# Performance work log

Hardware: AMD Instinct MI355X
Metric: run time of the kernel (lower is better)

Reference implementation:

```python
import jax, jax.numpy as jnp
import numpy as np

HIDDEN = 64
NHEADS = 8
HEAD_DIM = HIDDEN // NHEADS
N_EDGES = 800000
N_NODES = 50000


def setup_inputs() -> dict:
    key = jax.random.key(0)
    k1, k2, k3, k4 = jax.random.split(key, 4)
    keys = jax.random.normal(k1, (N_EDGES, HIDDEN), dtype=jnp.float32)
    queries = jax.random.normal(k2, (N_EDGES, HIDDEN), dtype=jnp.float32)
    values = jax.random.normal(k3, (N_EDGES, HIDDEN), dtype=jnp.float32)
    dst = jax.random.randint(k4, (N_EDGES,), 0, N_NODES, dtype=jnp.int32)
    return {"keys": keys, "queries": queries, "values": values,
            "dst": dst, "num_nodes": N_NODES}


def reference(keys, queries, values, dst, num_nodes):
    E = keys.shape[0]
    temp = HIDDEN ** (-0.5)
    # reshape to (E, H, D) multi-head layout
    k = keys.reshape(E, NHEADS, HEAD_DIM)
    q = queries.reshape(E, NHEADS, HEAD_DIM)
    v = values.reshape(E, NHEADS, HEAD_DIM)
    # edge-wise dot-product score per head, scaled, then LeakyReLU(0.2)
    scores = jnp.sum(k * q, axis=-1) * temp            # (E, H)
    scores = jnp.where(scores >= 0, scores, 0.2 * scores)
    # segment softmax over edges grouped by destination node (dgl.ops.edge_softmax)
    smax = jax.ops.segment_max(scores, dst, num_segments=num_nodes)  # (N, H)
    smax = jnp.where(jnp.isfinite(smax), smax, 0.0)    # nodes with no in-edges
    ex = jnp.exp(scores - smax[dst])                   # (E, H)
    denom = jax.ops.segment_sum(ex, dst, num_segments=num_nodes)    # (N, H)
    weights = ex / denom[dst]                          # (E, H)
    # dropout p=0.0 -> identity; mask/bias are None -> skipped
    weighted = weights[..., None] * v                  # (E, H, D)
    # scatter-sum to destination nodes (dgl.ops.copy_e_sum)
    out = jax.ops.segment_sum(weighted, dst, num_segments=num_nodes)  # (N, H, D)
    return out.reshape(num_nodes, HIDDEN)
```

## Files before the change

kernel.cpp:

```cpp
#include <hip/hip_runtime.h>

#define HIDDEN 64
#define NHEADS 8


__global__ void hist_kernel(const int* __restrict__ dst, int* __restrict__ counts, int E) {
    int i = blockIdx.x * blockDim.x + threadIdx.x;
    if (i < E) atomicAdd(&counts[dst[i]], 1);
}

__global__ void scan1_kernel(const int* __restrict__ counts, int* __restrict__ offsets,
                             int* __restrict__ partials, int N) {
    int tid = threadIdx.x, lane = tid & 63, wid = tid >> 6;
    int i = blockIdx.x * 256 + tid;
    int x0 = (i < N) ? counts[i] : 0;
    int x = x0;
    #pragma unroll
    for (int off = 1; off < 64; off <<= 1) {
        int y = __shfl_up(x, off);
        if (lane >= off) x += y;
    }
    __shared__ int wsum[4];
    if (lane == 63) wsum[wid] = x;
    __syncthreads();
    if (tid == 0) {
        int s = 0;
        #pragma unroll
        for (int w2 = 0; w2 < 4; ++w2) { int t = wsum[w2]; wsum[w2] = s; s += t; }
        partials[blockIdx.x] = s;
    }
    __syncthreads();
    if (i < N) offsets[i] = wsum[wid] + (x - x0);
}

__global__ void scan2_kernel(int* __restrict__ partials, int PB) {
    int tid = threadIdx.x, lane = tid & 63, wid = tid >> 6;
    int x0 = (tid < PB) ? partials[tid] : 0;
    int x = x0;
    #pragma unroll
    for (int off = 1; off < 64; off <<= 1) {
        int y = __shfl_up(x, off);
        if (lane >= off) x += y;
    }
    __shared__ int wsum[4];
    if (lane == 63) wsum[wid] = x;
    __syncthreads();
    if (tid == 0) {
        int s = 0;
        #pragma unroll
        for (int w2 = 0; w2 < 4; ++w2) { int t = wsum[w2]; wsum[w2] = s; s += t; }
    }
    __syncthreads();
    if (tid < PB) partials[tid] = wsum[wid] + (x - x0);
}

__global__ void scan3_kernel(int* __restrict__ offsets, int* __restrict__ cursor,
                             const int* __restrict__ partials, int N, int E) {
    int i = blockIdx.x * 256 + threadIdx.x;
    if (i < N) {
        int o = offsets[i] + partials[blockIdx.x];
        offsets[i] = o;
        cursor[i] = o;
    }
    if (i == 0) offsets[N] = E;
}

__global__ void scatter_kernel(const int* __restrict__ dst, int* __restrict__ cursor,
                               int* __restrict__ edge_ids, int E) {
    int i = blockIdx.x * blockDim.x + threadIdx.x;
    if (i < E) {
        int pos = atomicAdd(&cursor[dst[i]], 1);
        edge_ids[pos] = i;
    }
}

__global__ void score_kernel(const float* __restrict__ k,
                             const float* __restrict__ q,
                             float* __restrict__ ex_edge, int E) {
    int tid = blockIdx.x * blockDim.x + threadIdx.x;
    int e = tid >> 3, h = tid & 7;
    if (e >= E) return;

    const float4* kp = (const float4*)(k + (size_t)e * HIDDEN + h * 8);
    const float4* qp = (const float4*)(q + (size_t)e * HIDDEN + h * 8);
    float4 k0 = kp[0], k1 = kp[1];
    float4 q0 = qp[0], q1 = qp[1];
    float pr = k0.x * q0.x + k0.y * q0.y + k0.z * q0.z + k0.w * q0.w +
               k1.x * q1.x + k1.y * q1.y + k1.z * q1.z + k1.w * q1.w;
    float sc = pr * 0.125f;
    sc = (sc >= 0.f) ? sc : 0.2f * sc;
    ex_edge[tid] = __expf(sc);
}

__global__ void gat_gather_kernel(const float* __restrict__ v,
                                  const float* __restrict__ ex_edge,
                                  const int* __restrict__ offsets,
                                  const int* __restrict__ edge_ids,
                                  float* __restrict__ out, int N) {
    int wgid = blockIdx.x * (blockDim.x >> 6) + (threadIdx.x >> 6);
    if (wgid >= N) return;
    int lane = threadIdx.x & 63;
    int h = lane >> 3;
    int start = offsets[wgid], end = offsets[wgid + 1];
    if (end <= start) {
        out[(size_t)wgid * HIDDEN + lane] = 0.f;
        return;
    }
    float acc = 0.f, den = 0.f;

    for (int cbase = start; cbase < end; cbase += 16) {
        int idx[16];
        int eid[16];
        float w[16], vv[16];
        #pragma unroll
        for (int jj = 0; jj < 16; ++jj) {
            int i0 = cbase + jj;
            idx[jj] = (i0 < end) ? i0 : (end - 1);
        }
        #pragma unroll
        for (int jj = 0; jj < 16; ++jj) eid[jj] = edge_ids[idx[jj]];
        #pragma unroll
        for (int jj = 0; jj < 16; ++jj) {
            w[jj]  = ex_edge[(size_t)eid[jj] * 8 + h];
            vv[jj] = v[(size_t)eid[jj] * HIDDEN + lane];
        }
        #pragma unroll
        for (int jj = 0; jj < 16; ++jj) {
            float m = (cbase + jj < end) ? w[jj] : 0.f;
            acc = fmaf(m, vv[jj], acc);
            den += m;
        }
    }
    out[(size_t)wgid * HIDDEN + lane] = acc / den;
}

extern "C" void kernel_launch(void* const* d_in, const int* in_sizes, int n_in,
                              void* d_out, int out_size, void* d_ws, size_t ws_size,
                              hipStream_t stream) {
    const float* keys    = (const float*)d_in[0];
    const float* queries = (const float*)d_in[1];
    const float* values  = (const float*)d_in[2];
    const int*   dst     = (const int*)d_in[3];
    int E = in_sizes[0] / HIDDEN;
    int N = out_size / HIDDEN;

    int* counts   = (int*)d_ws;
    int* offsets  = counts + N;
    int* cursor   = offsets + N + 1;
    int* partials = cursor + N;
    int* edge_ids = partials + 256;
    float* ex_edge = (float*)(edge_ids + E);
    float* out    = (float*)d_out;

    hipMemsetAsync(counts, 0, (size_t)N * sizeof(int), stream);

    int threads = 256;
    int eb = (E + threads - 1) / threads;
    int nb256 = (N + 255) / 256;
    int ehb = ((E * NHEADS) + threads - 1) / threads;

    hist_kernel<<<eb, threads, 0, stream>>>(dst, counts, E);
    scan1_kernel<<<nb256, 256, 0, stream>>>(counts, offsets, partials, N);
    scan2_kernel<<<1, 256, 0, stream>>>(partials, nb256);
    scan3_kernel<<<nb256, 256, 0, stream>>>(offsets, cursor, partials, N, E);
    scatter_kernel<<<eb, threads, 0, stream>>>(dst, cursor, edge_ids, E);
    score_kernel<<<ehb, threads, 0, stream>>>(keys, queries, ex_edge, E);

    int wavesPerBlock = threads / 64;
    int gb = (N + wavesPerBlock - 1) / wavesPerBlock;
    gat_gather_kernel<<<gb, threads, 0, stream>>>(values, ex_edge, offsets,
                                                  edge_ids, out, N);
}
```

Before: 230.4 us.

## Coalesce score loads and permute edge weights into CSR order

```diff
diff --git a/kernel.cpp b/kernel.cpp
--- a/kernel.cpp
+++ b/kernel.cpp
@@ -78,22 +78,37 @@
                              const float* __restrict__ q,
                              float* __restrict__ ex_edge, int E) {
     int tid = blockIdx.x * blockDim.x + threadIdx.x;
-    int e = tid >> 3, h = tid & 7;
-    if (e >= E) return;
+    int total = E * 16;
+    int t = (tid < total) ? tid : (total - 1);
+    int lane = threadIdx.x & 63;
 
-    const float4* kp = (const float4*)(k + (size_t)e * HIDDEN + h * 8);
-    const float4* qp = (const float4*)(q + (size_t)e * HIDDEN + h * 8);
-    float4 k0 = kp[0], k1 = kp[1];
-    float4 q0 = qp[0], q1 = qp[1];
-    float pr = k0.x * q0.x + k0.y * q0.y + k0.z * q0.z + k0.w * q0.w +
-               k1.x * q1.x + k1.y * q1.y + k1.z * q1.z + k1.w * q1.w;
-    float sc = pr * 0.125f;
-    sc = (sc >= 0.f) ? sc : 0.2f * sc;
-    ex_edge[tid] = __expf(sc);
+    float4 kk = ((const float4*)k)[t];
+    float4 qq = ((const float4*)q)[t];
+    float pr = kk.x * qq.x + kk.y * qq.y + kk.z * qq.z + kk.w * qq.w;
+    pr += __shfl_xor(pr, 1);
+
+    float prs = __shfl(pr, (lane & 31) * 2);
+    int pair_base = (blockIdx.x * blockDim.x + (threadIdx.x & ~63)) >> 1;
+    int pidx = pair_base + (lane & 31);
+    if (lane < 32 && pidx < E * NHEADS) {
+        float sc = prs * 0.125f;
+        sc = (sc >= 0.f) ? sc : 0.2f * sc;
+        ex_edge[pidx] = __expf(sc);
+    }
+}
+
+__global__ void permute_ex_kernel(const float* __restrict__ ex_edge,
+                                  const int* __restrict__ edge_ids,
+                                  float* __restrict__ ex8, int E) {
+    int tid = blockIdx.x * blockDim.x + threadIdx.x;
+    if (tid >= E * 2) return;
+    int pos = tid >> 1, h4 = tid & 1;
+    int e = edge_ids[pos];
+    ((float4*)ex8)[tid] = ((const float4*)ex_edge)[(size_t)e * 2 + h4];
 }
 
 __global__ void gat_gather_kernel(const float* __restrict__ v,
-                                  const float* __restrict__ ex_edge,
+                                  const float* __restrict__ ex8,
                                   const int* __restrict__ offsets,
                                   const int* __restrict__ edge_ids,
                                   float* __restrict__ out, int N) {
@@ -121,7 +136,7 @@
         for (int jj = 0; jj < 16; ++jj) eid[jj] = edge_ids[idx[jj]];
         #pragma unroll
         for (int jj = 0; jj < 16; ++jj) {
-            w[jj]  = ex_edge[(size_t)eid[jj] * 8 + h];
+            w[jj]  = ex8[(size_t)idx[jj] * 8 + h];
             vv[jj] = v[(size_t)eid[jj] * HIDDEN + lane];
         }
         #pragma unroll
@@ -144,30 +159,35 @@
     int E = in_sizes[0] / HIDDEN;
     int N = out_size / HIDDEN;
 
-    int* counts   = (int*)d_ws;
-    int* offsets  = counts + N;
-    int* cursor   = offsets + N + 1;
-    int* partials = cursor + N;
-    int* edge_ids = partials + 256;
+    int* counts    = (int*)d_ws;
+    int* offsets   = counts + N;
+    int* cursor    = offsets + N + 1;
+    int* partials  = cursor + N;
+    int* edge_ids  = partials + 256;
     float* ex_edge = (float*)(edge_ids + E);
-    float* out    = (float*)d_out;
+    float* ex8     = ex_edge + (size_t)E * 8;
+    float* out     = (float*)d_out;
 
     hipMemsetAsync(counts, 0, (size_t)N * sizeof(int), stream);
 
     int threads = 256;
     int eb = (E + threads - 1) / threads;
     int nb256 = (N + 255) / 256;
-    int ehb = ((E * NHEADS) + threads - 1) / threads;
 
     hist_kernel<<<eb, threads, 0, stream>>>(dst, counts, E);
     scan1_kernel<<<nb256, 256, 0, stream>>>(counts, offsets, partials, N);
     scan2_kernel<<<1, 256, 0, stream>>>(partials, nb256);
     scan3_kernel<<<nb256, 256, 0, stream>>>(offsets, cursor, partials, N, E);
     scatter_kernel<<<eb, threads, 0, stream>>>(dst, cursor, edge_ids, E);
-    score_kernel<<<ehb, threads, 0, stream>>>(keys, queries, ex_edge, E);
+
+    int sb = ((E * 16) + threads - 1) / threads;
+    score_kernel<<<sb, threads, 0, stream>>>(keys, queries, ex_edge, E);
+
+    int pb = ((E * 2) + threads - 1) / threads;
+    permute_ex_kernel<<<pb, threads, 0, stream>>>(ex_edge, edge_ids, ex8, E);
 
     int wavesPerBlock = threads / 64;
     int gb = (N + wavesPerBlock - 1) / wavesPerBlock;
-    gat_gather_kernel<<<gb, threads, 0, stream>>>(values, ex_edge, offsets,
+    gat_gather_kernel<<<gb, threads, 0, stream>>>(values, ex8, offsets,
                                                   edge_ids, out, N);
 }
```

Measured after the change: 248.3 us. 7.8% more time.
